# Kernel tuning notes

Hardware: AMD Instinct MI355X
Metric: run time of the kernel (lower is better)

## Reference

```python
import jax, jax.numpy as jnp
import numpy as np

H = 16
D_MODEL = 1024
D_K = D_MODEL // H
NWORDS = 16384


def setup_inputs() -> dict:
    key0 = jax.random.key(0)
    ks = jax.random.split(key0, 11)
    s = 0.02
    return {
        "query": jax.random.normal(ks[0], (1, D_MODEL), dtype=jnp.float32),
        "key": jax.random.normal(ks[1], (NWORDS, D_MODEL), dtype=jnp.float32),
        "value": jax.random.normal(ks[2], (NWORDS, D_MODEL), dtype=jnp.float32),
        "Wq": jax.random.normal(ks[3], (D_MODEL, D_MODEL), dtype=jnp.float32) * s,
        "bq": jax.random.normal(ks[4], (D_MODEL,), dtype=jnp.float32) * s,
        "Wk": jax.random.normal(ks[5], (D_MODEL, D_MODEL), dtype=jnp.float32) * s,
        "bk": jax.random.normal(ks[6], (D_MODEL,), dtype=jnp.float32) * s,
        "Wv": jax.random.normal(ks[7], (D_MODEL, D_MODEL), dtype=jnp.float32) * s,
        "bv": jax.random.normal(ks[8], (D_MODEL,), dtype=jnp.float32) * s,
        "Wo": jax.random.normal(ks[9], (D_MODEL, D_MODEL), dtype=jnp.float32) * s,
        "bo": jax.random.normal(ks[10], (D_MODEL,), dtype=jnp.float32) * s,
    }


def reference(query, key, value, Wq, bq, Wk, bk, Wv, bv, Wo, bo):
    # torch Linear: y = x @ W.T + b
    q = (query @ Wq.T + bq).reshape(H, D_K)          # [h, d_k]  (single query token)
    k = (key @ Wk.T + bk).reshape(-1, H, D_K)        # [n, h, d_k]
    v = (value @ Wv.T + bv).reshape(-1, H, D_K)      # [n, h, d_k]
    # NOTE: original module applies NO 1/sqrt(d_k) scaling.
    scores = jnp.einsum("hd,nhd->hn", q, k)          # [h, n]
    p_attn = jax.nn.softmax(scores, axis=-1)          # dropout p=0 -> no-op
    x = jnp.einsum("hn,nhd->hd", p_attn, v).reshape(1, H * D_K)  # [1, d_model]
    return x @ Wo.T + bo                              # [1, d_model]
```

## Files before the change

### kernel.cpp

```cpp
#include <hip/hip_runtime.h>

#define DM 1024
#define NW 16384

typedef __attribute__((ext_vector_type(8))) short short8;
typedef __attribute__((ext_vector_type(4))) float f32x4;

#define OFF_AH   1024
#define OFF_AL   9216
#define OFF_D0   17408
#define OFF_SP   17440
#define OFF_X    25632
#define OFF_W    26656
#define OFF_PART 49152

__device__ __forceinline__ unsigned short f2bf(float f) {
  unsigned int u = __float_as_uint(f);
  return (unsigned short)((u + 0x7fffu + ((u >> 16) & 1u)) >> 16);
}

__device__ __forceinline__ void barrier_lgkm() {
  asm volatile("s_waitcnt lgkmcnt(0)" ::: "memory");
  __builtin_amdgcn_s_barrier();
  __builtin_amdgcn_sched_barrier(0);
}

__global__ __launch_bounds__(256) void k_rowdot(const float* __restrict__ W,
                                                const float* __restrict__ v,
                                                const float* __restrict__ b,
                                                float* __restrict__ out) {
  const int wave = (blockIdx.x * 256 + threadIdx.x) >> 6;
  const int lane = threadIdx.x & 63;
  const float* row = W + (size_t)wave * DM + 4 * lane;
  float s = 0.f;
#pragma unroll
  for (int j = 0; j < 4; ++j) {
    float4 a = *(const float4*)(row + j * 256);
    float4 x = *(const float4*)(v + j * 256 + 4 * lane);
    s += a.x * x.x + a.y * x.y + a.z * x.z + a.w * x.w;
  }
#pragma unroll
  for (int off = 32; off; off >>= 1) s += __shfl_xor(s, off, 64);
  if (lane == 0) out[wave] = s + b[wave];
}

__global__ __launch_bounds__(256) void k_qck(const float* __restrict__ Wq,
                                             const float* __restrict__ bq,
                                             const float* __restrict__ query,
                                             const float* __restrict__ Wk,
                                             const float* __restrict__ bk,
                                             short* __restrict__ Ah,
                                             short* __restrict__ Al,
                                             float* __restrict__ d0,
                                             float* __restrict__ w) {
  const int h = blockIdx.x >> 2;
  const int mc = blockIdx.x & 3;
  const int t = threadIdx.x;
  const int lane = t & 63;
  const int wv = t >> 6;
  __shared__ float qh[64];
  w[blockIdx.x * 256 + t] = 0.f;
  float4 qv[4];
#pragma unroll
  for (int j = 0; j < 4; ++j) qv[j] = *(const float4*)(query + j * 256 + 4 * lane);
#pragma unroll 1
  for (int ii = 0; ii < 16; ii += 4) {
    float4 a[4][4];
#pragma unroll
    for (int r = 0; r < 4; ++r) {
      const float* rp = Wq + (size_t)(h * 64 + 4 * (ii + r) + wv) * DM + 4 * lane;
#pragma unroll
      for (int j = 0; j < 4; ++j) a[r][j] = *(const float4*)(rp + j * 256);
    }
    float s[4] = {0.f, 0.f, 0.f, 0.f};
#pragma unroll
    for (int r = 0; r < 4; ++r)
#pragma unroll
      for (int j = 0; j < 4; ++j)
        s[r] += a[r][j].x * qv[j].x + a[r][j].y * qv[j].y +
                a[r][j].z * qv[j].z + a[r][j].w * qv[j].w;
#pragma unroll
    for (int off = 32; off; off >>= 1)
#pragma unroll
      for (int r = 0; r < 4; ++r) s[r] += __shfl_xor(s[r], off, 64);
    if (lane == 0)
#pragma unroll
      for (int r = 0; r < 4; ++r)
        qh[4 * (ii + r) + wv] = s[r] + bq[h * 64 + 4 * (ii + r) + wv];
  }
  __syncthreads();
  const int m = mc * 256 + t;
  const float* Wp = Wk + (size_t)(h * 64) * DM + m;
  float s = 0.f;
#pragma unroll 2
  for (int db = 0; db < 8; ++db) {
    float wv8[8];
#pragma unroll
    for (int j = 0; j < 8; ++j) wv8[j] = Wp[(size_t)(db * 8 + j) * DM];
#pragma unroll
    for (int j = 0; j < 8; ++j) s = fmaf(qh[db * 8 + j], wv8[j], s);
  }
  unsigned short hu = f2bf(s);
  float hf = __uint_as_float(((unsigned int)hu) << 16);
  unsigned short lu = f2bf(s - hf);
  const int kb = m >> 5, q = (m >> 3) & 3, j = m & 7;
  const int idx = (kb * 64 + q * 16 + h) * 8 + j;
  Ah[idx] = (short)hu;
  Al[idx] = (short)lu;
  if (mc == 0 && t == 0) {
    float tt = 0.f;
    for (int d = 0; d < 64; ++d) tt += qh[d] * bk[h * 64 + d];
    d0[h] = tt;
  }
}

__global__ __launch_bounds__(256, 2) void k_spv(const float* __restrict__ key,
                                                const float* __restrict__ value,
                                                const short* __restrict__ AhG,
                                                const short* __restrict__ AlG,
                                                const float* __restrict__ d0,
                                                float* __restrict__ part,
                                                float* __restrict__ Spart) {
  const int nb = blockIdx.x;
  const int t = threadIdx.x;
  const int lane = t & 63;
  const int wv = t >> 6;
  const int tile = wv >> 1;
  const int khalf = wv & 1;
  const int nl = tile * 16 + (lane & 15);
  const int n = nb * 32 + nl;
  const int quad = lane >> 4;
  const float* base = key + (size_t)n * DM + quad * 8;
  const short8* A8h = (const short8*)AhG;
  const short8* A8l = (const short8*)AlG;
  __shared__ float el[32 * 16];
  __shared__ f32x4 sred[4][64];

  short8 ah[3][4], al[3][4];
  float4 f0[3][4], f1[3][4];
  f32x4 acc0 = {0.f, 0.f, 0.f, 0.f};
  f32x4 acc1 = {0.f, 0.f, 0.f, 0.f};

#define LOADG(buf, g) { \
  _Pragma("unroll") for (int i = 0; i < 4; ++i) { \
    const int kb = khalf * 16 + (g) * 4 + i; \
    ah[buf][i] = A8h[kb * 64 + lane]; \
    al[buf][i] = A8l[kb * 64 + lane]; \
    f0[buf][i] = *(const float4*)(base + kb * 32); \
    f1[buf][i] = *(const float4*)(base + kb * 32 + 4); \
  } }

#define PROC(buf) { \
  _Pragma("unroll") for (int i = 0; i < 4; ++i) { \
    float ff[8] = {f0[buf][i].x, f0[buf][i].y, f0[buf][i].z, f0[buf][i].w, \
                   f1[buf][i].x, f1[buf][i].y, f1[buf][i].z, f1[buf][i].w}; \
    short8 bh, bl; \
    _Pragma("unroll") for (int j = 0; j < 8; ++j) { \
      unsigned short hu = f2bf(ff[j]); \
      bh[j] = (short)hu; \
      float hf = __uint_as_float(((unsigned int)hu) << 16); \
      bl[j] = (short)f2bf(ff[j] - hf); \
    } \
    if ((i & 1) == 0) { \
      acc0 = __builtin_amdgcn_mfma_f32_16x16x32_bf16(ah[buf][i], bh, acc0, 0, 0, 0); \
      acc0 = __builtin_amdgcn_mfma_f32_16x16x32_bf16(ah[buf][i], bl, acc0, 0, 0, 0); \
      acc0 = __builtin_amdgcn_mfma_f32_16x16x32_bf16(al[buf][i], bh, acc0, 0, 0, 0); \
    } else { \
      acc1 = __builtin_amdgcn_mfma_f32_16x16x32_bf16(ah[buf][i], bh, acc1, 0, 0, 0); \
      acc1 = __builtin_amdgcn_mfma_f32_16x16x32_bf16(ah[buf][i], bl, acc1, 0, 0, 0); \
      acc1 = __builtin_amdgcn_mfma_f32_16x16x32_bf16(al[buf][i], bh, acc1, 0, 0, 0); \
    } \
  } }

  LOADG(0, 0)
  LOADG(1, 1)
  LOADG(2, 2)
  PROC(0) LOADG(0, 3)
  PROC(1)
  PROC(2)
  PROC(0)
#undef LOADG
#undef PROC

  f32x4 at = acc0 + acc1;
  sred[wv][lane] = at;
  __syncthreads();
  if (khalf == 0) {
    f32x4 o = sred[wv + 1][lane];
    const float4 dv = *(const float4*)(d0 + quad * 4);
    float ex0 = __expf(at[0] + o[0] + dv.x);
    float ex1 = __expf(at[1] + o[1] + dv.y);
    float ex2 = __expf(at[2] + o[2] + dv.z);
    float ex3 = __expf(at[3] + o[3] + dv.w);
    *(float4*)&el[nl * 16 + quad * 4] = make_float4(ex0, ex1, ex2, ex3);
  }

  const float* vp = value + (size_t)(nb * 32) * DM + 4 * t;
  float4 vbuf[3][8];

#define LOADV(buf, g) { \
  _Pragma("unroll") for (int i = 0; i < 8; ++i) \
    vbuf[buf][i] = *(const float4*)(vp + (size_t)((g) * 8 + i) * DM); }

  LOADV(0, 0)
  barrier_lgkm();
  LOADV(1, 1)
  LOADV(2, 2)

  if (t < 16) {
    float s = 0.f;
#pragma unroll
    for (int r = 0; r < 32; ++r) s += el[r * 16 + t];
    Spart[t * 512 + nb] = s;
  }

  float4 acc[16];
#pragma unroll
  for (int h = 0; h < 16; ++h) acc[h] = make_float4(0.f, 0.f, 0.f, 0.f);

#define COMPV(buf, g) { \
  _Pragma("unroll") for (int i = 0; i < 8; ++i) { \
    const float4* er4 = (const float4*)&el[((g) * 8 + i) * 16]; \
    float4 e0 = er4[0], e1 = er4[1], e2 = er4[2], e3 = er4[3]; \
    float4 vvv = vbuf[buf][i]; \
    acc[0].x  = fmaf(e0.x, vvv.x, acc[0].x);  acc[0].y  = fmaf(e0.x, vvv.y, acc[0].y); \
    acc[0].z  = fmaf(e0.x, vvv.z, acc[0].z);  acc[0].w  = fmaf(e0.x, vvv.w, acc[0].w); \
    acc[1].x  = fmaf(e0.y, vvv.x, acc[1].x);  acc[1].y  = fmaf(e0.y, vvv.y, acc[1].y); \
    acc[1].z  = fmaf(e0.y, vvv.z, acc[1].z);  acc[1].w  = fmaf(e0.y, vvv.w, acc[1].w); \
    acc[2].x  = fmaf(e0.z, vvv.x, acc[2].x);  acc[2].y  = fmaf(e0.z, vvv.y, acc[2].y); \
    acc[2].z  = fmaf(e0.z, vvv.z, acc[2].z);  acc[2].w  = fmaf(e0.z, vvv.w, acc[2].w); \
    acc[3].x  = fmaf(e0.w, vvv.x, acc[3].x);  acc[3].y  = fmaf(e0.w, vvv.y, acc[3].y); \
    acc[3].z  = fmaf(e0.w, vvv.z, acc[3].z);  acc[3].w  = fmaf(e0.w, vvv.w, acc[3].w); \
    acc[4].x  = fmaf(e1.x, vvv.x, acc[4].x);  acc[4].y  = fmaf(e1.x, vvv.y, acc[4].y); \
    acc[4].z  = fmaf(e1.x, vvv.z, acc[4].z);  acc[4].w  = fmaf(e1.x, vvv.w, acc[4].w); \
    acc[5].x  = fmaf(e1.y, vvv.x, acc[5].x);  acc[5].y  = fmaf(e1.y, vvv.y, acc[5].y); \
    acc[5].z  = fmaf(e1.y, vvv.z, acc[5].z);  acc[5].w  = fmaf(e1.y, vvv.w, acc[5].w); \
    acc[6].x  = fmaf(e1.z, vvv.x, acc[6].x);  acc[6].y  = fmaf(e1.z, vvv.y, acc[6].y); \
    acc[6].z  = fmaf(e1.z, vvv.z, acc[6].z);  acc[6].w  = fmaf(e1.z, vvv.w, acc[6].w); \
    acc[7].x  = fmaf(e1.w, vvv.x, acc[7].x);  acc[7].y  = fmaf(e1.w, vvv.y, acc[7].y); \
    acc[7].z  = fmaf(e1.w, vvv.z, acc[7].z);  acc[7].w  = fmaf(e1.w, vvv.w, acc[7].w); \
    acc[8].x  = fmaf(e2.x, vvv.x, acc[8].x);  acc[8].y  = fmaf(e2.x, vvv.y, acc[8].y); \
    acc[8].z  = fmaf(e2.x, vvv.z, acc[8].z);  acc[8].w  = fmaf(e2.x, vvv.w, acc[8].w); \
    acc[9].x  = fmaf(e2.y, vvv.x, acc[9].x);  acc[9].y  = fmaf(e2.y, vvv.y, acc[9].y); \
    acc[9].z  = fmaf(e2.y, vvv.z, acc[9].z);  acc[9].w  = fmaf(e2.y, vvv.w, acc[9].w); \
    acc[10].x = fmaf(e2.z, vvv.x, acc[10].x); acc[10].y = fmaf(e2.z, vvv.y, acc[10].y); \
    acc[10].z = fmaf(e2.z, vvv.z, acc[10].z); acc[10].w = fmaf(e2.z, vvv.w, acc[10].w); \
    acc[11].x = fmaf(e2.w, vvv.x, acc[11].x); acc[11].y = fmaf(e2.w, vvv.y, acc[11].y); \
    acc[11].z = fmaf(e2.w, vvv.z, acc[11].z); acc[11].w = fmaf(e2.w, vvv.w, acc[11].w); \
    acc[12].x = fmaf(e3.x, vvv.x, acc[12].x); acc[12].y = fmaf(e3.x, vvv.y, acc[12].y); \
    acc[12].z = fmaf(e3.x, vvv.z, acc[12].z); acc[12].w = fmaf(e3.x, vvv.w, acc[12].w); \
    acc[13].x = fmaf(e3.y, vvv.x, acc[13].x); acc[13].y = fmaf(e3.y, vvv.y, acc[13].y); \
    acc[13].z = fmaf(e3.y, vvv.z, acc[13].z); acc[13].w = fmaf(e3.y, vvv.w, acc[13].w); \
    acc[14].x = fmaf(e3.z, vvv.x, acc[14].x); acc[14].y = fmaf(e3.z, vvv.y, acc[14].y); \
    acc[14].z = fmaf(e3.z, vvv.z, acc[14].z); acc[14].w = fmaf(e3.z, vvv.w, acc[14].w); \
    acc[15].x = fmaf(e3.w, vvv.x, acc[15].x); acc[15].y = fmaf(e3.w, vvv.y, acc[15].y); \
    acc[15].z = fmaf(e3.w, vvv.z, acc[15].z); acc[15].w = fmaf(e3.w, vvv.w, acc[15].w); \
  } }

  COMPV(0, 0) LOADV(0, 3)
  COMPV(1, 1)
  COMPV(2, 2)
  COMPV(0, 3)
#undef LOADV
#undef COMPV

  float* pp = part + (size_t)nb * (16 * DM) + 4 * t;
#pragma unroll
  for (int h = 0; h < 16; ++h) *(float4*)(pp + (size_t)h * DM) = acc[h];
}

__global__ __launch_bounds__(256) void k_wred(const float* __restrict__ part,
                                              float* __restrict__ w) {
  const int g = blockIdx.x * 256 + threadIdx.x;
  const int o = g & 16383;
  const int q = g >> 14;
  float s = 0.f;
#pragma unroll 1
  for (int ib = 0; ib < 16; ++ib) {
    float x[8];
#pragma unroll
    for (int j = 0; j < 8; ++j)
      x[j] = part[(size_t)(q * 128 + ib * 8 + j) * 16384 + o];
#pragma unroll
    for (int j = 0; j < 8; ++j) s += x[j];
  }
  atomicAdd(w + o, s);
}

__global__ __launch_bounds__(256) void k_xproj(const float* __restrict__ Wv,
                                               const float* __restrict__ w,
                                               const float* __restrict__ bv,
                                               const float* __restrict__ Spart,
                                               float* __restrict__ x) {
  const int wave = (blockIdx.x * 256 + threadIdx.x) >> 6;
  const int lane = threadIdx.x & 63;
  const int h = wave >> 6;
  const float* vec = w + (size_t)h * DM;
  const float* row = Wv + (size_t)wave * DM + 4 * lane;
  const float* sp = Spart + (size_t)h * 512;
  float s = 0.f, ss = 0.f;
#pragma unroll
  for (int i = 0; i < 8; ++i) ss += sp[i * 64 + lane];
#pragma unroll
  for (int j = 0; j < 4; ++j) {
    float4 a = *(const float4*)(row + j * 256);
    float4 x4 = *(const float4*)(vec + j * 256 + 4 * lane);
    s += a.x * x4.x + a.y * x4.y + a.z * x4.z + a.w * x4.w;
  }
#pragma unroll
  for (int off = 32; off; off >>= 1) {
    s += __shfl_xor(s, off, 64);
    ss += __shfl_xor(ss, off, 64);
  }
  if (lane == 0) x[wave] = s / ss + bv[wave];
}

extern "C" void kernel_launch(void* const* d_in, const int* in_sizes, int n_in,
                              void* d_out, int out_size, void* d_ws, size_t ws_size,
                              hipStream_t stream) {
  const float* query = (const float*)d_in[0];
  const float* key   = (const float*)d_in[1];
  const float* value = (const float*)d_in[2];
  const float* Wq    = (const float*)d_in[3];
  const float* bq    = (const float*)d_in[4];
  const float* Wk    = (const float*)d_in[5];
  const float* bk    = (const float*)d_in[6];
  const float* Wv    = (const float*)d_in[7];
  const float* bv    = (const float*)d_in[8];
  const float* Wo    = (const float*)d_in[9];
  const float* bo    = (const float*)d_in[10];
  float* out = (float*)d_out;
  float* ws  = (float*)d_ws;
  short* Ah  = (short*)(ws + OFF_AH);
  short* Al  = (short*)(ws + OFF_AL);

  k_qck    <<<64,  256, 0, stream>>>(Wq, bq, query, Wk, bk, Ah, Al,
                                     ws + OFF_D0, ws + OFF_W);
  k_spv    <<<512, 256, 0, stream>>>(key, value, Ah, Al, ws + OFF_D0,
                                     ws + OFF_PART, ws + OFF_SP);
  k_wred   <<<256, 256, 0, stream>>>(ws + OFF_PART, ws + OFF_W);
  k_xproj  <<<256, 256, 0, stream>>>(Wv, ws + OFF_W, bv, ws + OFF_SP, ws + OFF_X);
  k_rowdot <<<256, 256, 0, stream>>>(Wo, ws + OFF_X, bo, out);
}
```

Measured before the change: 208.8 us.

## Stage key tiles through swizzled shared memory with 512-thread blocks

The score kernel now uses 512 threads per block, with K split four ways across waves instead of two. Key rows are loaded cooperatively with coalesced float4 reads into a double-buffered, XOR-swizzled LDS tile, then read back for the bf16-split MFMA. Each thread handles two output columns instead of four in the value accumulation, which lowers register pressure and aims at higher occupancy. The cost is eight block barriers in the K loop and extra LDS traffic and footprint.

```diff
diff --git a/kernel.cpp b/kernel.cpp
--- a/kernel.cpp
+++ b/kernel.cpp
@@ -114,7 +114,7 @@
   }
 }
 
-__global__ __launch_bounds__(256, 2) void k_spv(const float* __restrict__ key,
+__global__ __launch_bounds__(512, 4) void k_spv(const float* __restrict__ key,
                                                 const float* __restrict__ value,
                                                 const short* __restrict__ AhG,
                                                 const short* __restrict__ AlG,
@@ -125,87 +125,107 @@
   const int t = threadIdx.x;
   const int lane = t & 63;
   const int wv = t >> 6;
-  const int tile = wv >> 1;
-  const int khalf = wv & 1;
-  const int nl = tile * 16 + (lane & 15);
-  const int n = nb * 32 + nl;
+  const int tile = wv >> 2;
+  const int kq = wv & 3;
+  const int row16 = lane & 15;
+  const int nl = tile * 16 + row16;
   const int quad = lane >> 4;
-  const float* base = key + (size_t)n * DM + quad * 8;
   const short8* A8h = (const short8*)AhG;
   const short8* A8l = (const short8*)AlG;
+
+  __shared__ float kbuf[2][32 * 128];
   __shared__ float el[32 * 16];
-  __shared__ f32x4 sred[4][64];
-
-  short8 ah[3][4], al[3][4];
-  float4 f0[3][4], f1[3][4];
+  __shared__ f32x4 sred[8][64];
+
+  const int srow0 = t >> 5;
+  const int srow1 = srow0 + 16;
+  const int c4 = t & 31;
+  const int st0 = srow0 * 128 + (((c4 << 4) ^ ((srow0 & 7) << 4)) >> 2);
+  const int st1 = srow1 * 128 + (((c4 << 4) ^ ((srow1 & 7) << 4)) >> 2);
+  const float* gs0 = key + (size_t)(nb * 32 + srow0) * DM + c4 * 4;
+  const float* gs1 = key + (size_t)(nb * 32 + srow1) * DM + c4 * 4;
+  const int swz = (row16 & 7) << 4;
+  const int rb0 = nl * 128 + (((kq * 128 + quad * 32) ^ swz) >> 2);
+  const int rb1 = nl * 128 + (((kq * 128 + quad * 32 + 16) ^ swz) >> 2);
+
   f32x4 acc0 = {0.f, 0.f, 0.f, 0.f};
   f32x4 acc1 = {0.f, 0.f, 0.f, 0.f};
-
-#define LOADG(buf, g) { \
-  _Pragma("unroll") for (int i = 0; i < 4; ++i) { \
-    const int kb = khalf * 16 + (g) * 4 + i; \
-    ah[buf][i] = A8h[kb * 64 + lane]; \
-    al[buf][i] = A8l[kb * 64 + lane]; \
-    f0[buf][i] = *(const float4*)(base + kb * 32); \
-    f1[buf][i] = *(const float4*)(base + kb * 32 + 4); \
-  } }
-
-#define PROC(buf) { \
-  _Pragma("unroll") for (int i = 0; i < 4; ++i) { \
-    float ff[8] = {f0[buf][i].x, f0[buf][i].y, f0[buf][i].z, f0[buf][i].w, \
-                   f1[buf][i].x, f1[buf][i].y, f1[buf][i].z, f1[buf][i].w}; \
-    short8 bh, bl; \
-    _Pragma("unroll") for (int j = 0; j < 8; ++j) { \
-      unsigned short hu = f2bf(ff[j]); \
-      bh[j] = (short)hu; \
-      float hf = __uint_as_float(((unsigned int)hu) << 16); \
-      bl[j] = (short)f2bf(ff[j] - hf); \
-    } \
-    if ((i & 1) == 0) { \
-      acc0 = __builtin_amdgcn_mfma_f32_16x16x32_bf16(ah[buf][i], bh, acc0, 0, 0, 0); \
-      acc0 = __builtin_amdgcn_mfma_f32_16x16x32_bf16(ah[buf][i], bl, acc0, 0, 0, 0); \
-      acc0 = __builtin_amdgcn_mfma_f32_16x16x32_bf16(al[buf][i], bh, acc0, 0, 0, 0); \
-    } else { \
-      acc1 = __builtin_amdgcn_mfma_f32_16x16x32_bf16(ah[buf][i], bh, acc1, 0, 0, 0); \
-      acc1 = __builtin_amdgcn_mfma_f32_16x16x32_bf16(ah[buf][i], bl, acc1, 0, 0, 0); \
-      acc1 = __builtin_amdgcn_mfma_f32_16x16x32_bf16(al[buf][i], bh, acc1, 0, 0, 0); \
-    } \
-  } }
-
-  LOADG(0, 0)
-  LOADG(1, 1)
-  LOADG(2, 2)
-  PROC(0) LOADG(0, 3)
-  PROC(1)
-  PROC(2)
-  PROC(0)
-#undef LOADG
-#undef PROC
+  float4 pa0, pa1, pb0, pb1;
+  short8 ahA, alA, ahB, alB;
+
+#define STAGE_LD(P0, P1, S) { P0 = *(const float4*)(gs0 + (S) * 128); \
+                              P1 = *(const float4*)(gs1 + (S) * 128); }
+#define A_LD(AH, AL, S) { AH = A8h[((S) * 4 + kq) * 64 + lane]; \
+                          AL = A8l[((S) * 4 + kq) * 64 + lane]; }
+#define DS_WR(B, P0, P1) { *(float4*)&kbuf[B][st0] = P0; \
+                           *(float4*)&kbuf[B][st1] = P1; }
+#define COMP(B, AH, AL, ACC) { \
+  float4 q0 = *(const float4*)&kbuf[B][rb0]; \
+  float4 q1 = *(const float4*)&kbuf[B][rb1]; \
+  float ff[8] = {q0.x, q0.y, q0.z, q0.w, q1.x, q1.y, q1.z, q1.w}; \
+  short8 bh, bl; \
+  _Pragma("unroll") for (int j = 0; j < 8; ++j) { \
+    unsigned short hu = f2bf(ff[j]); \
+    bh[j] = (short)hu; \
+    float hf = __uint_as_float(((unsigned int)hu) << 16); \
+    bl[j] = (short)f2bf(ff[j] - hf); \
+  } \
+  ACC = __builtin_amdgcn_mfma_f32_16x16x32_bf16(AH, bh, ACC, 0, 0, 0); \
+  ACC = __builtin_amdgcn_mfma_f32_16x16x32_bf16(AH, bl, ACC, 0, 0, 0); \
+  ACC = __builtin_amdgcn_mfma_f32_16x16x32_bf16(AL, bh, ACC, 0, 0, 0); }
+
+  STAGE_LD(pa0, pa1, 0) A_LD(ahA, alA, 0)
+  STAGE_LD(pb0, pb1, 1) A_LD(ahB, alB, 1)
+  DS_WR(0, pa0, pa1)
+  barrier_lgkm();
+  COMP(0, ahA, alA, acc0)
+  STAGE_LD(pa0, pa1, 2) A_LD(ahA, alA, 2)
+  DS_WR(1, pb0, pb1)
+  barrier_lgkm();
+  COMP(1, ahB, alB, acc1)
+  STAGE_LD(pb0, pb1, 3) A_LD(ahB, alB, 3)
+  DS_WR(0, pa0, pa1)
+  barrier_lgkm();
+  COMP(0, ahA, alA, acc0)
+  STAGE_LD(pa0, pa1, 4) A_LD(ahA, alA, 4)
+  DS_WR(1, pb0, pb1)
+  barrier_lgkm();
+  COMP(1, ahB, alB, acc1)
+  STAGE_LD(pb0, pb1, 5) A_LD(ahB, alB, 5)
+  DS_WR(0, pa0, pa1)
+  barrier_lgkm();
+  COMP(0, ahA, alA, acc0)
+  STAGE_LD(pa0, pa1, 6) A_LD(ahA, alA, 6)
+  DS_WR(1, pb0, pb1)
+  barrier_lgkm();
+  COMP(1, ahB, alB, acc1)
+  STAGE_LD(pb0, pb1, 7) A_LD(ahB, alB, 7)
+  DS_WR(0, pa0, pa1)
+  barrier_lgkm();
+  COMP(0, ahA, alA, acc0)
+  DS_WR(1, pb0, pb1)
+  barrier_lgkm();
+  COMP(1, ahB, alB, acc1)
+#undef STAGE_LD
+#undef A_LD
+#undef DS_WR
+#undef COMP
 
   f32x4 at = acc0 + acc1;
   sred[wv][lane] = at;
   __syncthreads();
-  if (khalf == 0) {
-    f32x4 o = sred[wv + 1][lane];
+  if (kq == 0) {
+    f32x4 o1 = sred[wv + 1][lane];
+    f32x4 o2 = sred[wv + 2][lane];
+    f32x4 o3 = sred[wv + 3][lane];
     const float4 dv = *(const float4*)(d0 + quad * 4);
-    float ex0 = __expf(at[0] + o[0] + dv.x);
-    float ex1 = __expf(at[1] + o[1] + dv.y);
-    float ex2 = __expf(at[2] + o[2] + dv.z);
-    float ex3 = __expf(at[3] + o[3] + dv.w);
+    float ex0 = __expf(at[0] + o1[0] + o2[0] + o3[0] + dv.x);
+    float ex1 = __expf(at[1] + o1[1] + o2[1] + o3[1] + dv.y);
+    float ex2 = __expf(at[2] + o1[2] + o2[2] + o3[2] + dv.z);
+    float ex3 = __expf(at[3] + o1[3] + o2[3] + o3[3] + dv.w);
     *(float4*)&el[nl * 16 + quad * 4] = make_float4(ex0, ex1, ex2, ex3);
   }
-
-  const float* vp = value + (size_t)(nb * 32) * DM + 4 * t;
-  float4 vbuf[3][8];
-
-#define LOADV(buf, g) { \
-  _Pragma("unroll") for (int i = 0; i < 8; ++i) \
-    vbuf[buf][i] = *(const float4*)(vp + (size_t)((g) * 8 + i) * DM); }
-
-  LOADV(0, 0)
-  barrier_lgkm();
-  LOADV(1, 1)
-  LOADV(2, 2)
+  __syncthreads();
 
   if (t < 16) {
     float s = 0.f;
@@ -214,59 +234,49 @@
     Spart[t * 512 + nb] = s;
   }
 
-  float4 acc[16];
-#pragma unroll
-  for (int h = 0; h < 16; ++h) acc[h] = make_float4(0.f, 0.f, 0.f, 0.f);
-
-#define COMPV(buf, g) { \
+  float2 acc[16];
+#pragma unroll
+  for (int h = 0; h < 16; ++h) acc[h] = make_float2(0.f, 0.f);
+  const float* vp = value + (size_t)(nb * 32) * DM + 2 * t;
+  float2 vbA[8], vbB[8];
+
+#define LOADV(VB, G) { _Pragma("unroll") for (int i = 0; i < 8; ++i) \
+    VB[i] = *(const float2*)(vp + (size_t)((G) * 8 + i) * DM); }
+#define COMPV(VB, G) { \
   _Pragma("unroll") for (int i = 0; i < 8; ++i) { \
-    const float4* er4 = (const float4*)&el[((g) * 8 + i) * 16]; \
+    const float4* er4 = (const float4*)&el[((G) * 8 + i) * 16]; \
     float4 e0 = er4[0], e1 = er4[1], e2 = er4[2], e3 = er4[3]; \
-    float4 vvv = vbuf[buf][i]; \
+    float2 vvv = VB[i]; \
     acc[0].x  = fmaf(e0.x, vvv.x, acc[0].x);  acc[0].y  = fmaf(e0.x, vvv.y, acc[0].y); \
-    acc[0].z  = fmaf(e0.x, vvv.z, acc[0].z);  acc[0].w  = fmaf(e0.x, vvv.w, acc[0].w); \
     acc[1].x  = fmaf(e0.y, vvv.x, acc[1].x);  acc[1].y  = fmaf(e0.y, vvv.y, acc[1].y); \
-    acc[1].z  = fmaf(e0.y, vvv.z, acc[1].z);  acc[1].w  = fmaf(e0.y, vvv.w, acc[1].w); \
     acc[2].x  = fmaf(e0.z, vvv.x, acc[2].x);  acc[2].y  = fmaf(e0.z, vvv.y, acc[2].y); \
-    acc[2].z  = fmaf(e0.z, vvv.z, acc[2].z);  acc[2].w  = fmaf(e0.z, vvv.w, acc[2].w); \
     acc[3].x  = fmaf(e0.w, vvv.x, acc[3].x);  acc[3].y  = fmaf(e0.w, vvv.y, acc[3].y); \
-    acc[3].z  = fmaf(e0.w, vvv.z, acc[3].z);  acc[3].w  = fmaf(e0.w, vvv.w, acc[3].w); \
     acc[4].x  = fmaf(e1.x, vvv.x, acc[4].x);  acc[4].y  = fmaf(e1.x, vvv.y, acc[4].y); \
-    acc[4].z  = fmaf(e1.x, vvv.z, acc[4].z);  acc[4].w  = fmaf(e1.x, vvv.w, acc[4].w); \
     acc[5].x  = fmaf(e1.y, vvv.x, acc[5].x);  acc[5].y  = fmaf(e1.y, vvv.y, acc[5].y); \
-    acc[5].z  = fmaf(e1.y, vvv.z, acc[5].z);  acc[5].w  = fmaf(e1.y, vvv.w, acc[5].w); \
     acc[6].x  = fmaf(e1.z, vvv.x, acc[6].x);  acc[6].y  = fmaf(e1.z, vvv.y, acc[6].y); \
-    acc[6].z  = fmaf(e1.z, vvv.z, acc[6].z);  acc[6].w  = fmaf(e1.z, vvv.w, acc[6].w); \
     acc[7].x  = fmaf(e1.w, vvv.x, acc[7].x);  acc[7].y  = fmaf(e1.w, vvv.y, acc[7].y); \
-    acc[7].z  = fmaf(e1.w, vvv.z, acc[7].z);  acc[7].w  = fmaf(e1.w, vvv.w, acc[7].w); \
     acc[8].x  = fmaf(e2.x, vvv.x, acc[8].x);  acc[8].y  = fmaf(e2.x, vvv.y, acc[8].y); \
-    acc[8].z  = fmaf(e2.x, vvv.z, acc[8].z);  acc[8].w  = fmaf(e2.x, vvv.w, acc[8].w); \
     acc[9].x  = fmaf(e2.y, vvv.x, acc[9].x);  acc[9].y  = fmaf(e2.y, vvv.y, acc[9].y); \
-    acc[9].z  = fmaf(e2.y, vvv.z, acc[9].z);  acc[9].w  = fmaf(e2.y, vvv.w, acc[9].w); \
     acc[10].x = fmaf(e2.z, vvv.x, acc[10].x); acc[10].y = fmaf(e2.z, vvv.y, acc[10].y); \
-    acc[10].z = fmaf(e2.z, vvv.z, acc[10].z); acc[10].w = fmaf(e2.z, vvv.w, acc[10].w); \
     acc[11].x = fmaf(e2.w, vvv.x, acc[11].x); acc[11].y = fmaf(e2.w, vvv.y, acc[11].y); \
-    acc[11].z = fmaf(e2.w, vvv.z, acc[11].z); acc[11].w = fmaf(e2.w, vvv.w, acc[11].w); \
     acc[12].x = fmaf(e3.x, vvv.x, acc[12].x); acc[12].y = fmaf(e3.x, vvv.y, acc[12].y); \
-    acc[12].z = fmaf(e3.x, vvv.z, acc[12].z); acc[12].w = fmaf(e3.x, vvv.w, acc[12].w); \
     acc[13].x = fmaf(e3.y, vvv.x, acc[13].x); acc[13].y = fmaf(e3.y, vvv.y, acc[13].y); \
-    acc[13].z = fmaf(e3.y, vvv.z, acc[13].z); acc[13].w = fmaf(e3.y, vvv.w, acc[13].w); \
     acc[14].x = fmaf(e3.z, vvv.x, acc[14].x); acc[14].y = fmaf(e3.z, vvv.y, acc[14].y); \
-    acc[14].z = fmaf(e3.z, vvv.z, acc[14].z); acc[14].w = fmaf(e3.z, vvv.w, acc[14].w); \
     acc[15].x = fmaf(e3.w, vvv.x, acc[15].x); acc[15].y = fmaf(e3.w, vvv.y, acc[15].y); \
-    acc[15].z = fmaf(e3.w, vvv.z, acc[15].z); acc[15].w = fmaf(e3.w, vvv.w, acc[15].w); \
   } }
 
-  COMPV(0, 0) LOADV(0, 3)
-  COMPV(1, 1)
-  COMPV(2, 2)
-  COMPV(0, 3)
+  LOADV(vbA, 0)
+  LOADV(vbB, 1)
+  COMPV(vbA, 0) LOADV(vbA, 2)
+  COMPV(vbB, 1) LOADV(vbB, 3)
+  COMPV(vbA, 2)
+  COMPV(vbB, 3)
 #undef LOADV
 #undef COMPV
 
-  float* pp = part + (size_t)nb * (16 * DM) + 4 * t;
-#pragma unroll
-  for (int h = 0; h < 16; ++h) *(float4*)(pp + (size_t)h * DM) = acc[h];
+  float* pp = part + (size_t)nb * (16 * DM) + 2 * t;
+#pragma unroll
+  for (int h = 0; h < 16; ++h) *(float2*)(pp + (size_t)h * DM) = acc[h];
 }
 
 __global__ __launch_bounds__(256) void k_wred(const float* __restrict__ part,
@@ -336,7 +346,7 @@
 
   k_qck    <<<64,  256, 0, stream>>>(Wq, bq, query, Wk, bk, Ah, Al,
                                      ws + OFF_D0, ws + OFF_W);
-  k_spv    <<<512, 256, 0, stream>>>(key, value, Ah, Al, ws + OFF_D0,
+  k_spv    <<<512, 512, 0, stream>>>(key, value, Ah, Al, ws + OFF_D0,
                                      ws + OFF_PART, ws + OFF_SP);
   k_wred   <<<256, 256, 0, stream>>>(ws + OFF_PART, ws + OFF_W);
   k_xproj  <<<256, 256, 0, stream>>>(Wv, ws + OFF_W, bv, ws + OFF_SP, ws + OFF_X);
```

Result: slower. 221.1 us (+5.9%).
